# Performance work log

Measured on AMD Instinct MI355X. Metric: run time of the kernel, lower is better.

## Reference

```python
import jax, jax.numpy as jnp
import numpy as np

MAX_N_LATENT = 8
EOS_THRESHOLD = 0.7
EOS_PATTERN_LEN = 3
COS_SIM_THRESHOLD = 0.3
EOS_SOFT_THRESHOLD = 0.5
CONTEXT_WINDOW = 2
EPS = 1e-8


def setup_inputs() -> dict:
    key = jax.random.key(0)
    k = jax.random.split(key, 8)
    B, S, D = 8, 4096, 1024
    s = 0.02
    latent_states = jax.random.normal(k[0], (B, S, D), dtype=jnp.float32)
    binary_mask = jax.random.randint(k[1], (B, S, 1), 0, 2).astype(jnp.int32)
    proj_w = jax.random.normal(k[2], (D, D), dtype=jnp.float32) * s
    proj_b = jax.random.normal(k[3], (D,), dtype=jnp.float32) * s
    eos_w1 = jax.random.normal(k[4], (D, D // 2), dtype=jnp.float32) * s
    eos_b1 = jax.random.normal(k[5], (D // 2,), dtype=jnp.float32) * s
    eos_w2 = jax.random.normal(k[6], (D // 2, 1), dtype=jnp.float32) * s
    eos_b2 = jax.random.normal(k[7], (1,), dtype=jnp.float32) * s
    return {"latent_states": latent_states, "binary_mask": binary_mask,
            "proj_w": proj_w, "proj_b": proj_b,
            "eos_w1": eos_w1, "eos_b1": eos_b1,
            "eos_w2": eos_w2, "eos_b2": eos_b2}


def reference(latent_states, binary_mask, proj_w, proj_b, eos_w1, eos_b1, eos_w2, eos_b2):
    B, S, D = latent_states.shape

    # ---- EOS scores (computed under no_grad in the original) ----
    h = jax.nn.relu(jnp.einsum('bsd,df->bsf', latent_states, eos_w1) + eos_b1)
    eos_scores = jax.nn.sigmoid(jnp.einsum('bsf,fo->bso', h, eos_w2) + eos_b2)[..., 0]
    eos_scores = jax.lax.stop_gradient(eos_scores)  # [B, S]

    # ---- segment ids: a boundary (mask==1) at i closes the patch that includes i ----
    m = binary_mask[..., 0].astype(jnp.int32)                 # [B, S]
    seg = jnp.cumsum(m, axis=1) - m                           # exclusive cumsum => patch id per token
    valid = (seg < MAX_N_LATENT).astype(latent_states.dtype)  # drop patches beyond MAX_N_LATENT (p[:max_patches])
    onehot = jax.nn.one_hot(jnp.clip(seg, 0, MAX_N_LATENT - 1), MAX_N_LATENT,
                            dtype=latent_states.dtype) * valid[..., None]  # [B, S, P]
    sums = jnp.einsum('bsp,bsd->bpd', onehot, latent_states)  # segmented sum
    counts = onehot.sum(axis=1)                               # [B, P]
    pooled = sums / jnp.maximum(counts, 1.0)[..., None]       # mean pooling; empty patches -> 0 (proj adds bias, as in torch)
    patches = jnp.einsum('bpd,do->bpo', pooled, proj_w) + proj_b  # [B, MAX_N_LATENT, output_dim]

    # ---- EOS bounds ----
    mthr = eos_scores > EOS_THRESHOLD
    run = mthr
    for t in range(1, EOS_PATTERN_LEN):                       # consecutive_eos_count >= EOS_PATTERN_LEN
        run = run & jnp.pad(mthr[:, :-t], ((0, 0), (t, 0)))
    a = latent_states[:, 1:-1]                                # prev state at i-1, for i >= 2
    b = latent_states[:, 2:]                                  # current state at i
    cos = (a * b).sum(-1) / (jnp.maximum(jnp.linalg.norm(a, axis=-1), EPS)
                             * jnp.maximum(jnp.linalg.norm(b, axis=-1), EPS))
    cos_rule = jnp.pad((cos < COS_SIM_THRESHOLD) & (eos_scores[:, 2:] > EOS_SOFT_THRESHOLD),
                       ((0, 0), (2, 0)))
    eos_any = run | cos_rule                                  # [B, S] (duplicate triggers don't change min/max)
    has = eos_any.any()
    idx = jnp.arange(S)[None, :]
    first = jnp.min(jnp.where(eos_any, idx, S))
    last = jnp.max(jnp.where(eos_any, idx, -1))
    start = jnp.maximum(0, first - CONTEXT_WINDOW)
    end = jnp.minimum(S - 1, last + CONTEXT_WINDOW)
    eos_bounds = jnp.where(has, jnp.stack([start, end]), jnp.full((2,), -1))
    return patches, eos_bounds
```

## Files before the change

kernel.cpp:

```cpp
#include <hip/hip_runtime.h>
#include <hip/hip_fp16.h>
#include <cstdint>
#include <cstddef>

#define B_ 8
#define S_ 4096
#define D_ 1024
#define H_ 512
#define M_ (B_*S_)

typedef __attribute__((ext_vector_type(8))) _Float16 half8;
typedef __attribute__((ext_vector_type(16))) float f16v;

union HU { int4 v; half8 h; };

__device__ inline unsigned short f2h(float f){
  _Float16 h = (_Float16)f;
  return __builtin_bit_cast(unsigned short, h);
}

__global__ __launch_bounds__(256) void k_pre(const float* __restrict__ X,
    float* __restrict__ n2o, float* __restrict__ dto, unsigned short* __restrict__ Xh,
    const float* __restrict__ w1, unsigned short* __restrict__ w1t,
    const int* __restrict__ mask, int* __restrict__ cb, float* __restrict__ logit,
    float* __restrict__ gsums, float* __restrict__ gcnt, int* __restrict__ fl){
  __shared__ float tile[32][33];
  __shared__ int sc[256];
  int bid = blockIdx.x, tid = threadIdx.x;
  if (bid < 512){
    int wave = tid>>6, lane = tid&63;
    int g0 = (bid*4 + wave)*16;
    const float4* Xv = (const float4*)X;
    ushort4* Xhv = (ushort4*)Xh;
    float4 pv[4];
    if ((g0 & (S_-1)) != 0){
      size_t bb = (size_t)(g0-1)*256;
      #pragma unroll
      for (int q=0;q<4;q++) pv[q] = Xv[bb + q*64 + lane];
    } else {
      #pragma unroll
      for (int q=0;q<4;q++) pv[q] = make_float4(0.f,0.f,0.f,0.f);
    }
    for (int r=0;r<16;r++){
      int g = g0 + r;
      size_t bb = (size_t)g*256;
      float4 cv[4];
      #pragma unroll
      for (int q=0;q<4;q++) cv[q] = Xv[bb + q*64 + lane];
      float n2=0.f, dp=0.f;
      #pragma unroll
      for (int q=0;q<4;q++){
        n2 += cv[q].x*cv[q].x + cv[q].y*cv[q].y + cv[q].z*cv[q].z + cv[q].w*cv[q].w;
        dp += pv[q].x*cv[q].x + pv[q].y*cv[q].y + pv[q].z*cv[q].z + pv[q].w*cv[q].w;
      }
      #pragma unroll
      for (int q=0;q<4;q++){
        ushort4 u;
        u.x = f2h(cv[q].x); u.y = f2h(cv[q].y); u.z = f2h(cv[q].z); u.w = f2h(cv[q].w);
        Xhv[bb + q*64 + lane] = u;
      }
      #pragma unroll
      for (int off=32; off>0; off>>=1){
        n2 += __shfl_down(n2, off);
        dp += __shfl_down(dp, off);
      }
      if (lane==0){
        n2o[g] = n2;
        if ((g & (S_-1)) != 0) dto[g-1] = dp;
      }
      #pragma unroll
      for (int q=0;q<4;q++) pv[q] = cv[q];
    }
  } else if (bid < 1024){
    int b = bid - 512;
    int n0 = (b&15)*32, k0 = (b>>4)*32;
    int tx = tid&31, ty = tid>>5;
    #pragma unroll
    for (int i=0;i<4;i++) tile[ty+8*i][tx] = w1[(size_t)(k0+ty+8*i)*H_ + n0+tx];
    __syncthreads();
    #pragma unroll
    for (int i=0;i<4;i++) w1t[(size_t)(n0+ty+8*i)*D_ + k0+tx] = f2h(tile[tx][ty+8*i]);
  } else {
    int bb = bid - 1024;
    const int* mrow = mask + (size_t)bb*S_ + tid*16;
    int s = 0;
    #pragma unroll
    for (int i=0;i<16;i++) s += mrow[i];
    sc[tid] = s;
    __syncthreads();
    for (int off=1; off<256; off<<=1){
      int v = (tid>=off) ? sc[tid-off] : 0;
      __syncthreads();
      sc[tid] += v;
      __syncthreads();
    }
    if ((tid & 15) == 0) cb[bb*16 + (tid>>4)] = (tid==0) ? 0 : sc[tid-1];
    float4* lz = (float4*)(logit + bb*4096);
    #pragma unroll
    for (int e=tid; e<1024; e+=256) lz[e] = make_float4(0.f,0.f,0.f,0.f);
    float4* gz = (float4*)(gsums + (size_t)bb*8192);
    for (int e=tid; e<2048; e+=256) gz[e] = make_float4(0.f,0.f,0.f,0.f);
    if (bb==0){
      if (tid < 64) gcnt[tid] = 0.f;
      if (tid == 64){ fl[0] = 0x7FFFFFFF; fl[1] = -1; fl[2] = 0; }
    }
  }
}

#define AS1 __attribute__((address_space(1)))
#define AS3 __attribute__((address_space(3)))

#define STAGE(kt_, nb_) do { int k0e = (kt_)*32; \
  char* abase = (char*)As[nb_]; char* bbase = (char*)Bs[nb_]; \
  _Pragma("unroll") for (int q=0;q<2;q++){ \
    __builtin_amdgcn_global_load_lds((const AS1 void*)(agp[q]+k0e), (AS3 void*)(abase+aldo[q]),16,0,0); \
    __builtin_amdgcn_global_load_lds((const AS1 void*)(bgp[q]+k0e), (AS3 void*)(bbase+bldo[q]),16,0,0); } \
} while(0)

__global__ __launch_bounds__(256) void k_mlp(const unsigned short* __restrict__ Xh,
    const unsigned short* __restrict__ W1T, const float* __restrict__ b1,
    const float* __restrict__ w2, float* __restrict__ logit){
  __shared__ __align__(16) unsigned short As[2][128*32];
  __shared__ __align__(16) unsigned short Bs[2][128*32];
  int tid = threadIdx.x;
  int wave = tid>>6, lane = tid&63;
  int l31 = lane&31, h = lane>>5;
  int m0 = (blockIdx.x>>2)*128, n0 = (blockIdx.x&3)*128;
  int wm = (wave>>1)*64, wn = (wave&1)*64;
  f16v acc[2][2] = {};

  int srow = lane>>2;
  const unsigned short* agp[2]; const unsigned short* bgp[2];
  unsigned aldo[2], bldo[2];
  #pragma unroll
  for (int q=0;q<2;q++){
    int rb = wave*32 + q*16;
    int r  = rb + srow;
    int c  = (lane&3) ^ ((r>>1)&3);
    agp[q] = Xh  + (size_t)(m0 + r)*D_ + c*8;
    bgp[q] = W1T + (size_t)(n0 + r)*D_ + c*8;
    aldo[q] = rb*64;
    bldo[q] = rb*64;
  }

  unsigned aoff[2][2], boff[2][2];
  #pragma unroll
  for (int i=0;i<2;i++){
    int rm = wm + 32*i + l31;
    int rn = wn + 32*i + l31;
    #pragma unroll
    for (int kk=0;kk<2;kk++){
      int c = kk*2 + h;
      aoff[i][kk] = rm*64 + ((c ^ ((rm>>1)&3))<<4);
      boff[i][kk] = rn*64 + ((c ^ ((rn>>1)&3))<<4);
    }
  }

  float b1v[2], w2v[2];
  #pragma unroll
  for (int j=0;j<2;j++){
    int n = n0 + wn + 32*j + l31;
    b1v[j] = b1[n]; w2v[j] = w2[n];
  }

  STAGE(0, 0);
  for (int kt=0; kt<32; ++kt){
    __syncthreads();
    if (kt < 31) STAGE(kt+1, (kt+1)&1);
    const char* ab = (const char*)As[kt&1];
    const char* bb = (const char*)Bs[kt&1];
    #pragma unroll
    for (int kk=0;kk<2;kk++){
      HU a0, a1, b0, b1u;
      a0.v  = *(const int4*)(ab + aoff[0][kk]);
      a1.v  = *(const int4*)(ab + aoff[1][kk]);
      b0.v  = *(const int4*)(bb + boff[0][kk]);
      b1u.v = *(const int4*)(bb + boff[1][kk]);
      acc[0][0] = __builtin_amdgcn_mfma_f32_32x32x16_f16(a0.h, b0.h,  acc[0][0], 0,0,0);
      acc[0][1] = __builtin_amdgcn_mfma_f32_32x32x16_f16(a0.h, b1u.h, acc[0][1], 0,0,0);
      acc[1][0] = __builtin_amdgcn_mfma_f32_32x32x16_f16(a1.h, b0.h,  acc[1][0], 0,0,0);
      acc[1][1] = __builtin_amdgcn_mfma_f32_32x32x16_f16(a1.h, b1u.h, acc[1][1], 0,0,0);
    }
  }

  #pragma unroll
  for (int i=0;i<2;i++){
    #pragma unroll
    for (int r=0;r<16;r++){
      float p = w2v[0]*fmaxf(acc[i][0][r] + b1v[0], 0.f)
              + w2v[1]*fmaxf(acc[i][1][r] + b1v[1], 0.f);
      p += __shfl_xor(p, 1);
      p += __shfl_xor(p, 2);
      p += __shfl_xor(p, 4);
      p += __shfl_xor(p, 8);
      p += __shfl_xor(p, 16);
      if (l31 == 0){
        int row = m0 + wm + 32*i + (r&3) + 8*(r>>2) + 4*h;
        atomicAdd(&logit[row], p);
      }
    }
  }
}

__global__ void k_pool(const float* __restrict__ X, const int* __restrict__ mask,
                       const int* __restrict__ cb, float* __restrict__ gsums,
                       float* __restrict__ gcnt){
  int c = blockIdx.x, b = blockIdx.y, tid = threadIdx.x;
  int base = cb[b*16 + c];
  if (base >= 8) return;
  __shared__ float lsum[8*1024];
  __shared__ int seg[256];
  __shared__ float lcnt[8];
  __shared__ int send_s;
  for (int e=tid; e<8192; e+=256) lsum[e] = 0.f;
  if (tid==0){
    float cnts[8] = {0,0,0,0,0,0,0,0};
    const int* mrow = mask + (size_t)b*S_ + c*256;
    int running = base, i = 0;
    for (; i<256; ++i){
      if (running >= 8) break;
      seg[i] = running;
      cnts[running] += 1.f;
      running += mrow[i];
    }
    send_s = i;
    #pragma unroll
    for (int p=0;p<8;p++) lcnt[p] = cnts[p];
  }
  __syncthreads();
  int send = send_s;
  for (int s2=0; s2<send; ++s2){
    int sg = seg[s2];
    size_t gb = ((size_t)(b*S_ + c*256 + s2))*D_;
    #pragma unroll
    for (int q=0;q<4;q++){
      int d = tid + q*256;
      lsum[sg*1024 + d] += X[gb + d];
    }
  }
  __syncthreads();
  for (int e=tid; e<8192; e+=256){
    float v = lsum[e];
    if (v != 0.f) atomicAdd(&gsums[(size_t)b*8192 + e], v);
  }
  if (tid < 8){
    float v = lcnt[tid];
    if (v != 0.f) atomicAdd(&gcnt[b*8 + tid], v);
  }
}

__global__ __launch_bounds__(256) void k_patch(const float* __restrict__ gsums,
                        const float* __restrict__ gcnt,
                        const float* __restrict__ pw, const float* __restrict__ pb,
                        float* __restrict__ out){
  __shared__ float pool[8192];
  __shared__ float red[2048];
  int b = blockIdx.y, cx = blockIdx.x, tid = threadIdx.x;
  const float4* gs4 = (const float4*)(gsums + (size_t)b*8192);
  float4* pool4 = (float4*)pool;
  for (int e4=tid; e4<2048; e4+=256){
    int p = e4>>8;
    float inv = 1.f / fmaxf(gcnt[b*8 + p], 1.f);
    float4 v = gs4[e4];
    v.x*=inv; v.y*=inv; v.z*=inv; v.w*=inv;
    pool4[e4] = v;
  }
  __syncthreads();
  int c = tid & 31, ks = tid >> 5;
  int col = cx*32 + c;
  float acc[8] = {0,0,0,0,0,0,0,0};
  for (int k=ks*128; k<ks*128+128; ++k){
    float w = pw[(size_t)k*D_ + col];
    #pragma unroll
    for (int p=0;p<8;p++) acc[p] += pool[p*1024 + k]*w;
  }
  #pragma unroll
  for (int p=0;p<8;p++) red[tid*8 + p] = acc[p];
  __syncthreads();
  {
    int p = tid>>5, cc = tid&31;
    float s = 0.f;
    #pragma unroll
    for (int k2=0;k2<8;k2++) s += red[(k2*32 + cc)*8 + p];
    out[(size_t)(b*8+p)*D_ + cx*32 + cc] = s + pb[cx*32 + cc];
  }
}

__global__ void k_flagsb(const float* __restrict__ logit, const float* __restrict__ n2,
                        const float* __restrict__ dt, const float* __restrict__ b2p,
                        int* __restrict__ fl, float* __restrict__ ob){
  int g = blockIdx.x*256 + threadIdx.x;
  float b2 = b2p[0];
  int s = g & (S_-1);
  bool any = false;
  if (s >= 2){
    float z0 = logit[g] + b2;
    float z1 = logit[g-1] + b2;
    float z2 = logit[g-2] + b2;
    const float THR = 0.8472978603872037f;
    bool run = (z0 > THR) & (z1 > THR) & (z2 > THR);
    float na = fmaxf(sqrtf(n2[g-1]), 1e-8f);
    float nb = fmaxf(sqrtf(n2[g]), 1e-8f);
    bool cosr = (dt[g-1] < 0.3f*na*nb) & (z0 > 0.f);
    any = run | cosr;
  }
  int mn = any ? s : 0x7FFFFFFF;
  int mx = any ? s : -1;
  #pragma unroll
  for (int off=32; off>0; off>>=1){
    mn = min(mn, __shfl_down(mn, off));
    mx = max(mx, __shfl_down(mx, off));
  }
  if ((threadIdx.x & 63) == 0){
    atomicMin(&fl[0], mn);
    atomicMax(&fl[1], mx);
  }
  __syncthreads();
  if (threadIdx.x == 0){
    __threadfence();
    int old = atomicAdd(&fl[2], 1);
    if (old == gridDim.x - 1){
      int f = atomicMin(&fl[0], 0x7FFFFFFF);
      int l = atomicMax(&fl[1], (int)0x80000000);
      if (l < 0){ ob[0] = -1.f; ob[1] = -1.f; }
      else {
        int st = f - 2; if (st < 0) st = 0;
        int en = l + 2; if (en > S_-1) en = S_-1;
        ob[0] = (float)st; ob[1] = (float)en;
      }
    }
  }
}

extern "C" void kernel_launch(void* const* d_in, const int* in_sizes, int n_in,
                              void* d_out, int out_size, void* d_ws, size_t ws_size,
                              hipStream_t stream){
  const float* latent = (const float*)d_in[0];
  const int*   mask   = (const int*)d_in[1];
  const float* proj_w = (const float*)d_in[2];
  const float* proj_b = (const float*)d_in[3];
  const float* eos_w1 = (const float*)d_in[4];
  const float* eos_b1 = (const float*)d_in[5];
  const float* eos_w2 = (const float*)d_in[6];
  const float* eos_b2 = (const float*)d_in[7];
  float* out = (float*)d_out;

  char* ws = (char*)d_ws;
  unsigned short* W1T = (unsigned short*)ws;
  unsigned short* Xh  = (unsigned short*)(ws + 1048576);
  float* fbase = (float*)(ws + 1048576 + 67108864);
  float* logit = fbase;
  float* norm2 = fbase + 32768;
  float* dotv  = fbase + 65536;
  float* gsums = fbase + 98304;
  float* gcnt  = fbase + 163840;
  int* chunkbase = (int*)(fbase + 163904);
  int* fl        = (int*)(fbase + 164032);

  k_pre<<<1032, 256, 0, stream>>>(latent, norm2, dotv, Xh, eos_w1, W1T, mask,
                                  chunkbase, logit, gsums, gcnt, fl);
  k_pool<<<dim3(16,8), 256, 0, stream>>>(latent, mask, chunkbase, gsums, gcnt);
  k_patch<<<dim3(32,8), 256, 0, stream>>>(gsums, gcnt, proj_w, proj_b, out);
  k_mlp<<<1024, 256, 0, stream>>>(Xh, W1T, eos_b1, eos_w2, logit);
  k_flagsb<<<128, 256, 0, stream>>>(logit, norm2, dotv, eos_b2, fl, out + 65536);
}
```

Before: 314.5 us.

## Fuse preprocessing, EOS MLP GEMM and flag reduction into one persistent kernel

Merges the preprocessing, MLP GEMM and EOS flag kernels into a single 1024-block kernel with software grid barriers implemented as atomic counters. Shared memory is unioned between the transpose/scan scratch and the GEMM tiles, and the zeroing work is split across blocks. The aim is to remove kernel launch gaps and tail effects between stages. It relies on all 1024 blocks being co-resident (launch bounds 256,4 on 256 CUs); otherwise the spin barrier would deadlock. The barrier waits add their own cost.

```diff
diff --git a/kernel.cpp b/kernel.cpp
--- a/kernel.cpp
+++ b/kernel.cpp
@@ -7,7 +7,7 @@
 #define S_ 4096
 #define D_ 1024
 #define H_ 512
-#define M_ (B_*S_)
+#define NBLK 1024
 
 typedef __attribute__((ext_vector_type(8))) _Float16 half8;
 typedef __attribute__((ext_vector_type(16))) float f16v;
@@ -19,17 +19,54 @@
   return __builtin_bit_cast(unsigned short, h);
 }
 
-__global__ __launch_bounds__(256) void k_pre(const float* __restrict__ X,
-    float* __restrict__ n2o, float* __restrict__ dto, unsigned short* __restrict__ Xh,
-    const float* __restrict__ w1, unsigned short* __restrict__ w1t,
-    const int* __restrict__ mask, int* __restrict__ cb, float* __restrict__ logit,
-    float* __restrict__ gsums, float* __restrict__ gcnt, int* __restrict__ fl){
-  __shared__ float tile[32][33];
-  __shared__ int sc[256];
+#define AS1 __attribute__((address_space(1)))
+#define AS3 __attribute__((address_space(3)))
+
+__global__ void k_init(int* sc, int* fl){
+  if (threadIdx.x == 0){
+    sc[0] = 0; sc[1] = 0;
+    fl[0] = 0x7FFFFFFF; fl[1] = -1; fl[2] = 0;
+  }
+}
+
+__device__ inline void gsync(int* c){
+  __syncthreads();
+  if (threadIdx.x == 0){
+    __threadfence();
+    __hip_atomic_fetch_add(c, 1, __ATOMIC_RELEASE, __HIP_MEMORY_SCOPE_AGENT);
+    while (__hip_atomic_load(c, __ATOMIC_RELAXED, __HIP_MEMORY_SCOPE_AGENT) < NBLK)
+      __builtin_amdgcn_s_sleep(32);
+    __threadfence();
+  }
+  __syncthreads();
+}
+
+union SMU {
+  struct { unsigned short A[2][4096]; unsigned short B[2][4096]; } g;
+  struct { float tile[32][33]; int sc[256]; } p;
+};
+
+#define STAGE(kt_, nb_) do { int k0e = (kt_)*32; \
+  char* abase = (char*)sm.g.A[nb_]; char* bbase = (char*)sm.g.B[nb_]; \
+  _Pragma("unroll") for (int q=0;q<2;q++){ \
+    __builtin_amdgcn_global_load_lds((const AS1 void*)(agp[q]+k0e), (AS3 void*)(abase+aldo[q]),16,0,0); \
+    __builtin_amdgcn_global_load_lds((const AS1 void*)(bgp[q]+k0e), (AS3 void*)(bbase+bldo[q]),16,0,0); } \
+} while(0)
+
+__global__ __launch_bounds__(256, 4) void k_mega(
+    const float* __restrict__ X, const int* __restrict__ mask,
+    const float* __restrict__ w1, const float* __restrict__ b1,
+    const float* __restrict__ w2, const float* __restrict__ b2p,
+    unsigned short* __restrict__ Xh, unsigned short* __restrict__ w1t,
+    float* __restrict__ n2o, float* __restrict__ dto, float* __restrict__ logit,
+    float* __restrict__ gsums, float* __restrict__ gcnt, int* __restrict__ cb,
+    int* __restrict__ fl, int* __restrict__ sc, float* __restrict__ ob){
+  __shared__ __align__(16) SMU sm;
   int bid = blockIdx.x, tid = threadIdx.x;
-  if (bid < 512){
-    int wave = tid>>6, lane = tid&63;
-    int g0 = (bid*4 + wave)*16;
+  int wave = tid>>6, lane = tid&63;
+
+  {
+    int g0 = bid*32 + wave*8;
     const float4* Xv = (const float4*)X;
     ushort4* Xhv = (ushort4*)Xh;
     float4 pv[4];
@@ -41,7 +78,7 @@
       #pragma unroll
       for (int q=0;q<4;q++) pv[q] = make_float4(0.f,0.f,0.f,0.f);
     }
-    for (int r=0;r<16;r++){
+    for (int r=0;r<8;r++){
       int g = g0 + r;
       size_t bb = (size_t)g*256;
       float4 cv[4];
@@ -71,132 +108,166 @@
       #pragma unroll
       for (int q=0;q<4;q++) pv[q] = cv[q];
     }
-  } else if (bid < 1024){
-    int b = bid - 512;
-    int n0 = (b&15)*32, k0 = (b>>4)*32;
+  }
+
+  if (bid < 512){
+    int n0 = (bid&15)*32, k0 = (bid>>4)*32;
     int tx = tid&31, ty = tid>>5;
-    #pragma unroll
-    for (int i=0;i<4;i++) tile[ty+8*i][tx] = w1[(size_t)(k0+ty+8*i)*H_ + n0+tx];
-    __syncthreads();
-    #pragma unroll
-    for (int i=0;i<4;i++) w1t[(size_t)(n0+ty+8*i)*D_ + k0+tx] = f2h(tile[tx][ty+8*i]);
-  } else {
-    int bb = bid - 1024;
+    __syncthreads();
+    #pragma unroll
+    for (int i=0;i<4;i++) sm.p.tile[ty+8*i][tx] = w1[(size_t)(k0+ty+8*i)*H_ + n0+tx];
+    __syncthreads();
+    #pragma unroll
+    for (int i=0;i<4;i++) w1t[(size_t)(n0+ty+8*i)*D_ + k0+tx] = f2h(sm.p.tile[tx][ty+8*i]);
+  } else if (bid < 520){
+    int bb = bid - 512;
     const int* mrow = mask + (size_t)bb*S_ + tid*16;
     int s = 0;
     #pragma unroll
     for (int i=0;i<16;i++) s += mrow[i];
-    sc[tid] = s;
+    __syncthreads();
+    sm.p.sc[tid] = s;
     __syncthreads();
     for (int off=1; off<256; off<<=1){
-      int v = (tid>=off) ? sc[tid-off] : 0;
+      int v = (tid>=off) ? sm.p.sc[tid-off] : 0;
       __syncthreads();
-      sc[tid] += v;
+      sm.p.sc[tid] += v;
       __syncthreads();
     }
-    if ((tid & 15) == 0) cb[bb*16 + (tid>>4)] = (tid==0) ? 0 : sc[tid-1];
-    float4* lz = (float4*)(logit + bb*4096);
-    #pragma unroll
-    for (int e=tid; e<1024; e+=256) lz[e] = make_float4(0.f,0.f,0.f,0.f);
-    float4* gz = (float4*)(gsums + (size_t)bb*8192);
-    for (int e=tid; e<2048; e+=256) gz[e] = make_float4(0.f,0.f,0.f,0.f);
-    if (bb==0){
-      if (tid < 64) gcnt[tid] = 0.f;
-      if (tid == 64){ fl[0] = 0x7FFFFFFF; fl[1] = -1; fl[2] = 0; }
-    }
-  }
-}
-
-#define AS1 __attribute__((address_space(1)))
-#define AS3 __attribute__((address_space(3)))
-
-#define STAGE(kt_, nb_) do { int k0e = (kt_)*32; \
-  char* abase = (char*)As[nb_]; char* bbase = (char*)Bs[nb_]; \
-  _Pragma("unroll") for (int q=0;q<2;q++){ \
-    __builtin_amdgcn_global_load_lds((const AS1 void*)(agp[q]+k0e), (AS3 void*)(abase+aldo[q]),16,0,0); \
-    __builtin_amdgcn_global_load_lds((const AS1 void*)(bgp[q]+k0e), (AS3 void*)(bbase+bldo[q]),16,0,0); } \
-} while(0)
-
-__global__ __launch_bounds__(256) void k_mlp(const unsigned short* __restrict__ Xh,
-    const unsigned short* __restrict__ W1T, const float* __restrict__ b1,
-    const float* __restrict__ w2, float* __restrict__ logit){
-  __shared__ __align__(16) unsigned short As[2][128*32];
-  __shared__ __align__(16) unsigned short Bs[2][128*32];
-  int tid = threadIdx.x;
-  int wave = tid>>6, lane = tid&63;
-  int l31 = lane&31, h = lane>>5;
-  int m0 = (blockIdx.x>>2)*128, n0 = (blockIdx.x&3)*128;
-  int wm = (wave>>1)*64, wn = (wave&1)*64;
-  f16v acc[2][2] = {};
-
-  int srow = lane>>2;
-  const unsigned short* agp[2]; const unsigned short* bgp[2];
-  unsigned aldo[2], bldo[2];
-  #pragma unroll
-  for (int q=0;q<2;q++){
-    int rb = wave*32 + q*16;
-    int r  = rb + srow;
-    int c  = (lane&3) ^ ((r>>1)&3);
-    agp[q] = Xh  + (size_t)(m0 + r)*D_ + c*8;
-    bgp[q] = W1T + (size_t)(n0 + r)*D_ + c*8;
-    aldo[q] = rb*64;
-    bldo[q] = rb*64;
-  }
-
-  unsigned aoff[2][2], boff[2][2];
-  #pragma unroll
-  for (int i=0;i<2;i++){
-    int rm = wm + 32*i + l31;
-    int rn = wn + 32*i + l31;
-    #pragma unroll
-    for (int kk=0;kk<2;kk++){
-      int c = kk*2 + h;
-      aoff[i][kk] = rm*64 + ((c ^ ((rm>>1)&3))<<4);
-      boff[i][kk] = rn*64 + ((c ^ ((rn>>1)&3))<<4);
-    }
-  }
-
-  float b1v[2], w2v[2];
-  #pragma unroll
-  for (int j=0;j<2;j++){
-    int n = n0 + wn + 32*j + l31;
-    b1v[j] = b1[n]; w2v[j] = w2[n];
-  }
-
-  STAGE(0, 0);
-  for (int kt=0; kt<32; ++kt){
-    __syncthreads();
-    if (kt < 31) STAGE(kt+1, (kt+1)&1);
-    const char* ab = (const char*)As[kt&1];
-    const char* bb = (const char*)Bs[kt&1];
-    #pragma unroll
-    for (int kk=0;kk<2;kk++){
-      HU a0, a1, b0, b1u;
-      a0.v  = *(const int4*)(ab + aoff[0][kk]);
-      a1.v  = *(const int4*)(ab + aoff[1][kk]);
-      b0.v  = *(const int4*)(bb + boff[0][kk]);
-      b1u.v = *(const int4*)(bb + boff[1][kk]);
-      acc[0][0] = __builtin_amdgcn_mfma_f32_32x32x16_f16(a0.h, b0.h,  acc[0][0], 0,0,0);
-      acc[0][1] = __builtin_amdgcn_mfma_f32_32x32x16_f16(a0.h, b1u.h, acc[0][1], 0,0,0);
-      acc[1][0] = __builtin_amdgcn_mfma_f32_32x32x16_f16(a1.h, b0.h,  acc[1][0], 0,0,0);
-      acc[1][1] = __builtin_amdgcn_mfma_f32_32x32x16_f16(a1.h, b1u.h, acc[1][1], 0,0,0);
-    }
-  }
-
-  #pragma unroll
-  for (int i=0;i<2;i++){
-    #pragma unroll
-    for (int r=0;r<16;r++){
-      float p = w2v[0]*fmaxf(acc[i][0][r] + b1v[0], 0.f)
-              + w2v[1]*fmaxf(acc[i][1][r] + b1v[1], 0.f);
-      p += __shfl_xor(p, 1);
-      p += __shfl_xor(p, 2);
-      p += __shfl_xor(p, 4);
-      p += __shfl_xor(p, 8);
-      p += __shfl_xor(p, 16);
-      if (l31 == 0){
-        int row = m0 + wm + 32*i + (r&3) + 8*(r>>2) + 4*h;
-        atomicAdd(&logit[row], p);
+    if ((tid & 15) == 0) cb[bb*16 + (tid>>4)] = (tid==0) ? 0 : sm.p.sc[tid-1];
+  } else if (bid < 552){
+    ((float4*)logit)[(bid-520)*256 + tid] = make_float4(0.f,0.f,0.f,0.f);
+  } else if (bid < 616){
+    ((float4*)gsums)[(bid-552)*256 + tid] = make_float4(0.f,0.f,0.f,0.f);
+  } else if (bid == 616){
+    if (tid < 64) gcnt[tid] = 0.f;
+  }
+
+  gsync(sc + 0);
+
+  {
+    int l31 = lane&31, h = lane>>5;
+    int m0 = (bid>>2)*128, n0 = (bid&3)*128;
+    int wm = (wave>>1)*64, wn = (wave&1)*64;
+    f16v acc[2][2] = {};
+
+    int srow = lane>>2;
+    const unsigned short* agp[2]; const unsigned short* bgp[2];
+    unsigned aldo[2], bldo[2];
+    #pragma unroll
+    for (int q=0;q<2;q++){
+      int rb = wave*32 + q*16;
+      int r  = rb + srow;
+      int c  = (lane&3) ^ ((r>>1)&3);
+      agp[q] = Xh  + (size_t)(m0 + r)*D_ + c*8;
+      bgp[q] = w1t + (size_t)(n0 + r)*D_ + c*8;
+      aldo[q] = rb*64;
+      bldo[q] = rb*64;
+    }
+
+    unsigned aoff[2][2], boff[2][2];
+    #pragma unroll
+    for (int i=0;i<2;i++){
+      int rm = wm + 32*i + l31;
+      int rn = wn + 32*i + l31;
+      #pragma unroll
+      for (int kk=0;kk<2;kk++){
+        int c = kk*2 + h;
+        aoff[i][kk] = rm*64 + ((c ^ ((rm>>1)&3))<<4);
+        boff[i][kk] = rn*64 + ((c ^ ((rn>>1)&3))<<4);
+      }
+    }
+
+    float b1v[2], w2v[2];
+    #pragma unroll
+    for (int j=0;j<2;j++){
+      int n = n0 + wn + 32*j + l31;
+      b1v[j] = b1[n]; w2v[j] = w2[n];
+    }
+
+    STAGE(0, 0);
+    for (int kt=0; kt<32; ++kt){
+      __syncthreads();
+      if (kt < 31) STAGE(kt+1, (kt+1)&1);
+      const char* ab = (const char*)sm.g.A[kt&1];
+      const char* bb = (const char*)sm.g.B[kt&1];
+      #pragma unroll
+      for (int kk=0;kk<2;kk++){
+        HU a0, a1, b0, b1u;
+        a0.v  = *(const int4*)(ab + aoff[0][kk]);
+        a1.v  = *(const int4*)(ab + aoff[1][kk]);
+        b0.v  = *(const int4*)(bb + boff[0][kk]);
+        b1u.v = *(const int4*)(bb + boff[1][kk]);
+        acc[0][0] = __builtin_amdgcn_mfma_f32_32x32x16_f16(a0.h, b0.h,  acc[0][0], 0,0,0);
+        acc[0][1] = __builtin_amdgcn_mfma_f32_32x32x16_f16(a0.h, b1u.h, acc[0][1], 0,0,0);
+        acc[1][0] = __builtin_amdgcn_mfma_f32_32x32x16_f16(a1.h, b0.h,  acc[1][0], 0,0,0);
+        acc[1][1] = __builtin_amdgcn_mfma_f32_32x32x16_f16(a1.h, b1u.h, acc[1][1], 0,0,0);
+      }
+    }
+
+    #pragma unroll
+    for (int i=0;i<2;i++){
+      #pragma unroll
+      for (int r=0;r<16;r++){
+        float p = w2v[0]*fmaxf(acc[i][0][r] + b1v[0], 0.f)
+                + w2v[1]*fmaxf(acc[i][1][r] + b1v[1], 0.f);
+        p += __shfl_xor(p, 1);
+        p += __shfl_xor(p, 2);
+        p += __shfl_xor(p, 4);
+        p += __shfl_xor(p, 8);
+        p += __shfl_xor(p, 16);
+        if (l31 == 0){
+          int row = m0 + wm + 32*i + (r&3) + 8*(r>>2) + 4*h;
+          atomicAdd(&logit[row], p);
+        }
+      }
+    }
+  }
+
+  gsync(sc + 1);
+
+  {
+    float b2 = b2p[0];
+    if (tid < 32){
+      int g = bid*32 + tid;
+      int s = g & (S_-1);
+      bool any = false;
+      if (s >= 2){
+        float z0 = logit[g] + b2;
+        float z1 = logit[g-1] + b2;
+        float z2 = logit[g-2] + b2;
+        const float THR = 0.8472978603872037f;
+        bool run = (z0 > THR) & (z1 > THR) & (z2 > THR);
+        float na = fmaxf(sqrtf(n2o[g-1]), 1e-8f);
+        float nb = fmaxf(sqrtf(n2o[g]), 1e-8f);
+        bool cosr = (dto[g-1] < 0.3f*na*nb) & (z0 > 0.f);
+        any = run | cosr;
+      }
+      int mn = any ? s : 0x7FFFFFFF;
+      int mx = any ? s : -1;
+      #pragma unroll
+      for (int off=16; off>0; off>>=1){
+        mn = min(mn, __shfl_down(mn, off, 32));
+        mx = max(mx, __shfl_down(mx, off, 32));
+      }
+      if (tid == 0){
+        atomicMin(&fl[0], mn);
+        atomicMax(&fl[1], mx);
+      }
+    }
+    __syncthreads();
+    if (tid == 0){
+      __threadfence();
+      int old = atomicAdd(&fl[2], 1);
+      if (old == NBLK - 1){
+        int f = atomicMin(&fl[0], 0x7FFFFFFF);
+        int l = atomicMax(&fl[1], (int)0x80000000);
+        if (l < 0){ ob[0] = -1.f; ob[1] = -1.f; }
+        else {
+          int st = f - 2; if (st < 0) st = 0;
+          int en = l + 2; if (en > S_-1) en = S_-1;
+          ob[0] = (float)st; ob[1] = (float)en;
+        }
       }
     }
   }
@@ -286,52 +357,6 @@
   }
 }
 
-__global__ void k_flagsb(const float* __restrict__ logit, const float* __restrict__ n2,
-                        const float* __restrict__ dt, const float* __restrict__ b2p,
-                        int* __restrict__ fl, float* __restrict__ ob){
-  int g = blockIdx.x*256 + threadIdx.x;
-  float b2 = b2p[0];
-  int s = g & (S_-1);
-  bool any = false;
-  if (s >= 2){
-    float z0 = logit[g] + b2;
-    float z1 = logit[g-1] + b2;
-    float z2 = logit[g-2] + b2;
-    const float THR = 0.8472978603872037f;
-    bool run = (z0 > THR) & (z1 > THR) & (z2 > THR);
-    float na = fmaxf(sqrtf(n2[g-1]), 1e-8f);
-    float nb = fmaxf(sqrtf(n2[g]), 1e-8f);
-    bool cosr = (dt[g-1] < 0.3f*na*nb) & (z0 > 0.f);
-    any = run | cosr;
-  }
-  int mn = any ? s : 0x7FFFFFFF;
-  int mx = any ? s : -1;
-  #pragma unroll
-  for (int off=32; off>0; off>>=1){
-    mn = min(mn, __shfl_down(mn, off));
-    mx = max(mx, __shfl_down(mx, off));
-  }
-  if ((threadIdx.x & 63) == 0){
-    atomicMin(&fl[0], mn);
-    atomicMax(&fl[1], mx);
-  }
-  __syncthreads();
-  if (threadIdx.x == 0){
-    __threadfence();
-    int old = atomicAdd(&fl[2], 1);
-    if (old == gridDim.x - 1){
-      int f = atomicMin(&fl[0], 0x7FFFFFFF);
-      int l = atomicMax(&fl[1], (int)0x80000000);
-      if (l < 0){ ob[0] = -1.f; ob[1] = -1.f; }
-      else {
-        int st = f - 2; if (st < 0) st = 0;
-        int en = l + 2; if (en > S_-1) en = S_-1;
-        ob[0] = (float)st; ob[1] = (float)en;
-      }
-    }
-  }
-}
-
 extern "C" void kernel_launch(void* const* d_in, const int* in_sizes, int n_in,
                               void* d_out, int out_size, void* d_ws, size_t ws_size,
                               hipStream_t stream){
@@ -356,11 +381,12 @@
   float* gcnt  = fbase + 163840;
   int* chunkbase = (int*)(fbase + 163904);
   int* fl        = (int*)(fbase + 164032);
-
-  k_pre<<<1032, 256, 0, stream>>>(latent, norm2, dotv, Xh, eos_w1, W1T, mask,
-                                  chunkbase, logit, gsums, gcnt, fl);
+  int* sc        = (int*)(fbase + 164035);
+
+  k_init<<<1, 64, 0, stream>>>(sc, fl);
+  k_mega<<<NBLK, 256, 0, stream>>>(latent, mask, eos_w1, eos_b1, eos_w2, eos_b2,
+                                   Xh, W1T, norm2, dotv, logit, gsums, gcnt,
+                                   chunkbase, fl, sc, out + 65536);
   k_pool<<<dim3(16,8), 256, 0, stream>>>(latent, mask, chunkbase, gsums, gcnt);
   k_patch<<<dim3(32,8), 256, 0, stream>>>(gsums, gcnt, proj_w, proj_b, out);
-  k_mlp<<<1024, 256, 0, stream>>>(Xh, W1T, eos_b1, eos_w2, logit);
-  k_flagsb<<<128, 256, 0, stream>>>(logit, norm2, dotv, eos_b2, fl, out + 65536);
-}
+}
```

Result: slower. 613.4 us (+95.1%).
